# Kernel optimization log

Hardware: AMD Instinct MI355X
Metric: run time of the kernel (lower is better)

The kernel has to match this reference:

```python
import jax, jax.numpy as jnp
import numpy as np
import math

H = 16
D_MODEL = 1024
D_K = D_MODEL // H


def setup_inputs() -> dict:
    key = jax.random.key(0)
    ks = jax.random.split(key, 12)
    B, S = 4, 2048
    inp = {
        "query": jax.random.normal(ks[0], (B, S, D_MODEL), jnp.float32),
        "key": jax.random.normal(ks[1], (B, S, D_MODEL), jnp.float32),
        "value": jax.random.normal(ks[2], (B, S, D_MODEL), jnp.float32),
        # causal mask, broadcastable over heads: [B, 1, S, S]
        "mask": jnp.broadcast_to(jnp.tril(jnp.ones((S, S), bool)), (B, 1, S, S)),
    }
    sc = 1.0 / math.sqrt(D_MODEL)
    inp["Wq"] = jax.random.normal(ks[3], (D_MODEL, D_MODEL), jnp.float32) * sc
    inp["bq"] = jnp.zeros((D_MODEL,), jnp.float32)
    inp["Wk"] = jax.random.normal(ks[4], (D_MODEL, D_MODEL), jnp.float32) * sc
    inp["bk"] = jnp.zeros((D_MODEL,), jnp.float32)
    inp["Wv"] = jax.random.normal(ks[5], (D_MODEL, D_MODEL), jnp.float32) * sc
    inp["bv"] = jnp.zeros((D_MODEL,), jnp.float32)
    inp["Wo"] = jax.random.normal(ks[6], (D_MODEL, D_MODEL), jnp.float32) * sc
    inp["bo"] = jnp.zeros((D_MODEL,), jnp.float32)
    return inp


def reference(query, key, value, mask, Wq, bq, Wk, bk, Wv, bv, Wo, bo):
    B, S, D = query.shape
    # torch nn.Linear: y = x @ W.T + b; then view(B,-1,h,d_k).transpose(1,2)
    def proj(x, W, b):
        return (x @ W.T + b).reshape(B, -1, H, D_K).transpose(0, 2, 1, 3)  # [B,h,S,d_k]

    q = proj(query, Wq, bq)
    k = proj(key, Wk, bk)
    v = proj(value, Wv, bv)

    scores = jnp.einsum("bhqd,bhkd->bhqk", q, k) / math.sqrt(D_K)
    scores = jnp.where(mask, scores, jnp.finfo(scores.dtype).min)
    p_attn = jax.nn.softmax(scores, axis=-1)  # dropout: eval mode (identity)
    x = jnp.einsum("bhqk,bhkd->bhqd", p_attn, v)
    x = x.transpose(0, 2, 1, 3).reshape(B, -1, H * D_K)
    return x @ Wo.T + bo
```

## Files before the change

kernel.cpp:

```cpp
#include <hip/hip_runtime.h>
#include <hip/hip_bf16.h>

typedef unsigned short u16;
typedef unsigned int u32;
typedef __attribute__((ext_vector_type(8))) short short8;
typedef __attribute__((ext_vector_type(4))) short short4v;
typedef __attribute__((ext_vector_type(4))) float f32x4;
typedef __attribute__((ext_vector_type(4))) float float4_t;

#define DIM 1024
#define NH  16
#define DKK 64
#define SEQ 2048
#define NB  4
#define SM_SCALE 0.1803368801111244f

__device__ __forceinline__ u16 f2bf(float f) {
    __bf16 h = (__bf16)f;
    return __builtin_bit_cast(u16, h);
}

__device__ __forceinline__ f32x4 mfma_bf16(short8 a, short8 b, f32x4 c) {
    return __builtin_amdgcn_mfma_f32_16x16x32_bf16(a, b, c, 0, 0, 0);
}

__device__ __forceinline__ short8 pack8(float4_t a, float4_t b) {
    short8 v;
    v[0] = (short)f2bf(a[0]); v[1] = (short)f2bf(a[1]);
    v[2] = (short)f2bf(a[2]); v[3] = (short)f2bf(a[3]);
    v[4] = (short)f2bf(b[0]); v[5] = (short)f2bf(b[1]);
    v[6] = (short)f2bf(b[2]); v[7] = (short)f2bf(b[3]);
    return v;
}

typedef const __attribute__((address_space(1))) u32* gas1_t;
typedef __attribute__((address_space(3))) u32* las3_t;
__device__ __forceinline__ void g2l16(const void* g, void* l) {
    __builtin_amdgcn_global_load_lds((gas1_t)g, (las3_t)l, 16, 0, 0);
}

template<int MODE>
__global__ __launch_bounds__(256)
void gemm128(const float* __restrict__ Afp, const u16* __restrict__ Abf,
             const float* __restrict__ W, const float* __restrict__ bias,
             u16* __restrict__ Cbf, float* __restrict__ Cf)
{
    __shared__ __align__(16) char AsRaw[MODE == 1 ? 8192 : 16384];
    __shared__ __align__(16) float Bs[128 * 32];

    const int tid  = threadIdx.x;
    const int lane = tid & 63;
    const int w    = tid >> 6;
    const int wr   = w >> 1, wc = w & 1;
    const int m0   = blockIdx.y * 128;
    const int n0   = blockIdx.x * 128;
    const int lm   = lane & 15, lg = lane >> 4;

    const int fr = tid >> 3;
    const int fc = (tid & 7) ^ ((tid >> 3) & 7);
    const int hr = tid >> 2;
    const int hc = (tid & 3) ^ ((tid >> 3) & 3);

    f32x4 acc[4][4];
#pragma unroll
    for (int i = 0; i < 4; ++i)
#pragma unroll
        for (int j = 0; j < 4; ++j) acc[i][j] = (f32x4){0.f, 0.f, 0.f, 0.f};

    for (int k0 = 0; k0 < DIM; k0 += 32) {
        __syncthreads();
        if (MODE == 1) {
#pragma unroll
            for (int c = 0; c < 2; ++c)
                g2l16(Abf + (size_t)(m0 + c * 64 + hr) * DIM + k0 + hc * 8,
                      AsRaw + c * 4096 + w * 1024);
        } else {
#pragma unroll
            for (int c = 0; c < 4; ++c)
                g2l16(Afp + (size_t)(m0 + c * 32 + fr) * DIM + k0 + fc * 4,
                      AsRaw + c * 4096 + w * 1024);
        }
#pragma unroll
        for (int c = 0; c < 4; ++c)
            g2l16(W + (size_t)(n0 + c * 32 + fr) * DIM + k0 + fc * 4,
                  (char*)Bs + c * 4096 + w * 1024);
        __syncthreads();

        short8 af[4], bfr[4];
#pragma unroll
        for (int t = 0; t < 4; ++t) {
            {
                const int R = wc * 64 + t * 16 + lm;
                const float* rowp = Bs + R * 32;
                const int sw = lm & 7;
                const float4_t fa = *(const float4_t*)(rowp + ((((lg * 2)    ) ^ sw) << 2));
                const float4_t fb = *(const float4_t*)(rowp + ((((lg * 2) | 1) ^ sw) << 2));
                bfr[t] = pack8(fa, fb);
            }
            const int R = wr * 64 + t * 16 + lm;
            if (MODE == 1) {
                const u16* Ash = (const u16*)AsRaw;
                const int ch = lg ^ ((lm >> 1) & 3);
                af[t] = *(const short8*)(Ash + R * 32 + ch * 8);
            } else {
                const float* Asf = (const float*)AsRaw;
                const float* rowp = Asf + R * 32;
                const int sw = lm & 7;
                const float4_t fa = *(const float4_t*)(rowp + ((((lg * 2)    ) ^ sw) << 2));
                const float4_t fb = *(const float4_t*)(rowp + ((((lg * 2) | 1) ^ sw) << 2));
                af[t] = pack8(fa, fb);
            }
        }
#pragma unroll
        for (int mt = 0; mt < 4; ++mt)
#pragma unroll
            for (int nt = 0; nt < 4; ++nt)
                acc[mt][nt] = mfma_bf16(af[mt], bfr[nt], acc[mt][nt]);
    }

#pragma unroll
    for (int mt = 0; mt < 4; ++mt)
#pragma unroll
        for (int nt = 0; nt < 4; ++nt)
#pragma unroll
            for (int r = 0; r < 4; ++r) {
                const int m = m0 + wr * 64 + mt * 16 + lg * 4 + r;
                const int n = n0 + wc * 64 + nt * 16 + lm;
                if (MODE == 0) {
                    const float val = acc[mt][nt][r] + bias[n];
                    const int b = m >> 11, s = m & 2047;
                    const int h = n >> 6,  dk = n & 63;
                    Cbf[(((size_t)b * NH + h) * SEQ + s) * DKK + dk] = f2bf(val);
                } else if (MODE == 1) {
                    Cf[(size_t)m * DIM + n] = acc[mt][nt][r] + bias[n];
                } else {
                    const float val = acc[mt][nt][r] + bias[m];
                    const int h = m >> 6, dk = m & 63;
                    const int b = n >> 11, s = n & 2047;
                    Cbf[(((size_t)b * NH + h) * DKK + dk) * SEQ + s] = f2bf(val);
                }
            }
}

__global__ __launch_bounds__(256, 2)
void attn3(const u16* __restrict__ Q, const u16* __restrict__ K,
           const u16* __restrict__ Vt, u16* __restrict__ O)
{
    __shared__ __align__(16) u16 Ks[64][72];
    __shared__ __align__(16) u16 Vs[64][72];
    __shared__ __align__(16) u16 Ps[4][32][72];

    const int tid  = threadIdx.x;
    const int lane = tid & 63;
    const int w    = tid >> 6;
    const int lm   = lane & 15, lg = lane >> 4;
    const int Lr   = blockIdx.y * gridDim.x + blockIdx.x;
    const int work = (Lr & 7) * 128 + (Lr >> 3);
    const int pb   = work & 15;
    const int bh   = work >> 4;
    const int Abase = pb * 64;
    const int Bbase = SEQ - 64 - Abase;
    const int qA = Abase + 16 * w;
    const int qB = Bbase + 16 * w;
    const u16* Qp = Q  + (size_t)bh * SEQ * DKK;
    const u16* Kp = K  + (size_t)bh * SEQ * DKK;
    const u16* Vp = Vt + (size_t)bh * DKK * SEQ;

    short8 qa[2][2];
#pragma unroll
    for (int kh = 0; kh < 2; ++kh) {
        qa[0][kh] = *(const short8*)(Qp + (size_t)(qA + lm) * DKK + kh * 32 + lg * 8);
        qa[1][kh] = *(const short8*)(Qp + (size_t)(qB + lm) * DKK + kh * 32 + lg * 8);
    }

    float m_q[2] = {-INFINITY, -INFINITY};
    float l_q[2] = {0.f, 0.f};
    f32x4 o[2][4];
#pragma unroll
    for (int qt = 0; qt < 2; ++qt)
#pragma unroll
        for (int dt = 0; dt < 4; ++dt) o[qt][dt] = (f32x4){0.f, 0.f, 0.f, 0.f};

    const f32x4 zero = (f32x4){0.f, 0.f, 0.f, 0.f};
    const int srow = tid >> 3;
    const int soct = (tid & 7) * 8;
    const int kv_end = Bbase + 64;

    short8 rk0 = *(const short8*)(Kp + (size_t)srow * DKK + soct);
    short8 rk1 = *(const short8*)(Kp + (size_t)(srow + 32) * DKK + soct);
    short8 rv0 = *(const short8*)(Vp + (size_t)srow * SEQ + soct);
    short8 rv1 = *(const short8*)(Vp + (size_t)(srow + 32) * SEQ + soct);

    for (int kv0 = 0; kv0 < kv_end; kv0 += 64) {
        __syncthreads();
        *(short8*)&Ks[srow][soct]      = rk0;
        *(short8*)&Ks[srow + 32][soct] = rk1;
        *(short8*)&Vs[srow][soct]      = rv0;
        *(short8*)&Vs[srow + 32][soct] = rv1;
        const int nkv = kv0 + 64;
        if (nkv < kv_end) {
            rk0 = *(const short8*)(Kp + (size_t)(nkv + srow) * DKK + soct);
            rk1 = *(const short8*)(Kp + (size_t)(nkv + srow + 32) * DKK + soct);
            rv0 = *(const short8*)(Vp + (size_t)srow * SEQ + nkv + soct);
            rv1 = *(const short8*)(Vp + (size_t)(srow + 32) * SEQ + nkv + soct);
        }
        __syncthreads();

        const bool actA = kv0 < qA + 16;
        const bool msk[2] = { kv0 + 63 > qA, kv0 + 63 > qB };
        const bool act[2] = { actA, true };
        const int  qb[2]  = { qA, qB };

        f32x4 s[2][4];
#pragma unroll
        for (int kvt = 0; kvt < 4; ++kvt) {
            const short8 kb0 = *(const short8*)&Ks[kvt * 16 + lm][lg * 8];
            const short8 kb1 = *(const short8*)&Ks[kvt * 16 + lm][32 + lg * 8];
            s[1][kvt] = mfma_bf16(kb1, qa[1][1], mfma_bf16(kb0, qa[1][0], zero));
            if (actA)
                s[0][kvt] = mfma_bf16(kb1, qa[0][1], mfma_bf16(kb0, qa[0][0], zero));
        }

        float mx[2] = {-INFINITY, -INFINITY};
#pragma unroll
        for (int qt = 0; qt < 2; ++qt) {
            if (!act[qt]) continue;
#pragma unroll
            for (int kvt = 0; kvt < 4; ++kvt)
#pragma unroll
                for (int r = 0; r < 4; ++r) s[qt][kvt][r] *= SM_SCALE;
            if (msk[qt]) {
                const int q = qb[qt] + lm;
#pragma unroll
                for (int kvt = 0; kvt < 4; ++kvt)
#pragma unroll
                    for (int r = 0; r < 4; ++r) {
                        const int kv = kv0 + kvt * 16 + lg * 4 + r;
                        if (kv > q) s[qt][kvt][r] = -INFINITY;
                    }
            }
            float vmax = -INFINITY;
#pragma unroll
            for (int kvt = 0; kvt < 4; ++kvt)
#pragma unroll
                for (int r = 0; r < 4; ++r) vmax = fmaxf(vmax, s[qt][kvt][r]);
            vmax = fmaxf(vmax, __shfl_xor(vmax, 16));
            vmax = fmaxf(vmax, __shfl_xor(vmax, 32));
            mx[qt] = vmax;
        }

        const bool small = (!actA || mx[0] <= m_q[0] + 8.f) && (mx[1] <= m_q[1] + 8.f);
        if (__all(small)) {
#pragma unroll
            for (int qt = 0; qt < 2; ++qt) {
                if (!act[qt]) continue;
                float ls = 0.f;
#pragma unroll
                for (int kvt = 0; kvt < 4; ++kvt) {
                    short4v pk;
#pragma unroll
                    for (int r = 0; r < 4; ++r) {
                        const float p = __builtin_exp2f(s[qt][kvt][r] - m_q[qt]);
                        ls += p;
                        pk[r] = (short)f2bf(p);
                    }
                    *(short4v*)&Ps[w][qt * 16 + lm][kvt * 16 + lg * 4] = pk;
                }
                l_q[qt] += ls;
            }
        } else {
#pragma unroll
            for (int qt = 0; qt < 2; ++qt) {
                if (!act[qt]) continue;
                const float mnew = fmaxf(m_q[qt], mx[qt]);
                const float alpha = __builtin_exp2f(m_q[qt] - mnew);
                m_q[qt] = mnew;
                float ls = 0.f;
#pragma unroll
                for (int kvt = 0; kvt < 4; ++kvt) {
                    short4v pk;
#pragma unroll
                    for (int r = 0; r < 4; ++r) {
                        const float p = __builtin_exp2f(s[qt][kvt][r] - mnew);
                        ls += p;
                        pk[r] = (short)f2bf(p);
                    }
                    *(short4v*)&Ps[w][qt * 16 + lm][kvt * 16 + lg * 4] = pk;
                }
                l_q[qt] = l_q[qt] * alpha + ls;
#pragma unroll
                for (int r = 0; r < 4; ++r) {
                    const float ar = __shfl(alpha, lg * 4 + r);
#pragma unroll
                    for (int dt = 0; dt < 4; ++dt) o[qt][dt][r] *= ar;
                }
            }
        }
        asm volatile("s_waitcnt lgkmcnt(0)" ::: "memory");

        short8 pa[2][2], vbt[4][2];
#pragma unroll
        for (int qt = 0; qt < 2; ++qt)
            if (act[qt]) {
                pa[qt][0] = *(const short8*)&Ps[w][qt * 16 + lm][lg * 8];
                pa[qt][1] = *(const short8*)&Ps[w][qt * 16 + lm][32 + lg * 8];
            }
#pragma unroll
        for (int dt = 0; dt < 4; ++dt) {
            vbt[dt][0] = *(const short8*)&Vs[dt * 16 + lm][lg * 8];
            vbt[dt][1] = *(const short8*)&Vs[dt * 16 + lm][32 + lg * 8];
        }
#pragma unroll
        for (int dt = 0; dt < 4; ++dt)
#pragma unroll
            for (int qt = 0; qt < 2; ++qt) {
                if (!act[qt]) continue;
                o[qt][dt] = mfma_bf16(pa[qt][1], vbt[dt][1],
                                      mfma_bf16(pa[qt][0], vbt[dt][0], o[qt][dt]));
            }
    }

    const int b = bh >> 4, h = bh & 15;
#pragma unroll
    for (int qt = 0; qt < 2; ++qt) {
        float lf = l_q[qt];
        lf += __shfl_xor(lf, 16);
        lf += __shfl_xor(lf, 32);
        const int qbase = qt ? qB : qA;
#pragma unroll
        for (int r = 0; r < 4; ++r) {
            const float li = 1.f / __shfl(lf, lg * 4 + r);
            const int srw = qbase + lg * 4 + r;
#pragma unroll
            for (int dt = 0; dt < 4; ++dt)
                O[(((size_t)b * SEQ + srw) * NH + h) * DKK + dt * 16 + lm] =
                    f2bf(o[qt][dt][r] * li);
        }
    }
}

extern "C" void kernel_launch(void* const* d_in, const int* in_sizes, int n_in,
                              void* d_out, int out_size, void* d_ws, size_t ws_size,
                              hipStream_t stream)
{
    const float* query = (const float*)d_in[0];
    const float* key   = (const float*)d_in[1];
    const float* value = (const float*)d_in[2];
    const float* Wq = (const float*)d_in[4];
    const float* bq = (const float*)d_in[5];
    const float* Wk = (const float*)d_in[6];
    const float* bk = (const float*)d_in[7];
    const float* Wv = (const float*)d_in[8];
    const float* bv = (const float*)d_in[9];
    const float* Wo = (const float*)d_in[10];
    const float* bo = (const float*)d_in[11];
    float* out = (float*)d_out;

    const size_t HD = (size_t)NB * NH * SEQ * DKK;
    u16* qws  = (u16*)d_ws;
    u16* kws  = qws + HD;
    u16* vtws = kws + HD;
    u16* ows  = vtws + HD;

    dim3 gg(DIM / 128, (NB * SEQ) / 128);
    dim3 gv((NB * SEQ) / 128, DIM / 128);
    gemm128<0><<<gg, 256, 0, stream>>>(query, nullptr, Wq, bq, qws, nullptr);
    gemm128<0><<<gg, 256, 0, stream>>>(key,   nullptr, Wk, bk, kws, nullptr);
    gemm128<2><<<gv, 256, 0, stream>>>(Wv, nullptr, value, bv, vtws, nullptr);
    attn3<<<dim3(16, NB * NH), 256, 0, stream>>>(qws, kws, vtws, ows);
    gemm128<1><<<gg, 256, 0, stream>>>(nullptr, ows, Wo, bo, nullptr, out);
}
```

Before: 264.6 us.

## Pre-convert inputs and weights to bf16 before GEMMs and fold softmax scale into Q

```diff
diff --git a/kernel.cpp b/kernel.cpp
--- a/kernel.cpp
+++ b/kernel.cpp
@@ -39,15 +39,43 @@
     __builtin_amdgcn_global_load_lds((gas1_t)g, (las3_t)l, 16, 0, 0);
 }
 
+__device__ __forceinline__ float max16(const f32x4* s) {
+    const float a = fmaxf(fmaxf(s[0][0], s[0][1]), fmaxf(s[0][2], s[0][3]));
+    const float b = fmaxf(fmaxf(s[1][0], s[1][1]), fmaxf(s[1][2], s[1][3]));
+    const float c = fmaxf(fmaxf(s[2][0], s[2][1]), fmaxf(s[2][2], s[2][3]));
+    const float d = fmaxf(fmaxf(s[3][0], s[3][1]), fmaxf(s[3][2], s[3][3]));
+    return fmaxf(fmaxf(a, b), fmaxf(c, d));
+}
+
+__global__ __launch_bounds__(256) void conv8(const float* __restrict__ src,
+                                             u16* __restrict__ dst) {
+    const int i = (blockIdx.x * 256 + threadIdx.x) * 8;
+    const float4_t a = *(const float4_t*)(src + i);
+    const float4_t b = *(const float4_t*)(src + i + 4);
+    *(short8*)(dst + i) = pack8(a, b);
+}
+
+__global__ __launch_bounds__(256) void conv8w(const float* __restrict__ w0,
+                                              const float* __restrict__ w1,
+                                              const float* __restrict__ w2,
+                                              const float* __restrict__ w3,
+                                              u16* __restrict__ dst) {
+    const int t = blockIdx.y;
+    const float* s = t == 0 ? w0 : t == 1 ? w1 : t == 2 ? w2 : w3;
+    const int i = (blockIdx.x * 256 + threadIdx.x) * 8;
+    const float4_t a = *(const float4_t*)(s + i);
+    const float4_t b = *(const float4_t*)(s + i + 4);
+    *(short8*)(dst + (size_t)t * DIM * DIM + i) = pack8(a, b);
+}
+
 template<int MODE>
 __global__ __launch_bounds__(256)
-void gemm128(const float* __restrict__ Afp, const u16* __restrict__ Abf,
-             const float* __restrict__ W, const float* __restrict__ bias,
-             u16* __restrict__ Cbf, float* __restrict__ Cf)
+void gemmb(const u16* __restrict__ A, const u16* __restrict__ Bw,
+           const float* __restrict__ bias, float scale,
+           u16* __restrict__ Cbf, float* __restrict__ Cf)
 {
-    __shared__ __align__(16) char AsRaw[MODE == 1 ? 8192 : 16384];
-    __shared__ __align__(16) float Bs[128 * 32];
-
+    __shared__ __align__(16) u16 As[128][32];
+    __shared__ __align__(16) u16 Bs[128][32];
     const int tid  = threadIdx.x;
     const int lane = tid & 63;
     const int w    = tid >> 6;
@@ -55,11 +83,8 @@
     const int m0   = blockIdx.y * 128;
     const int n0   = blockIdx.x * 128;
     const int lm   = lane & 15, lg = lane >> 4;
-
-    const int fr = tid >> 3;
-    const int fc = (tid & 7) ^ ((tid >> 3) & 7);
-    const int hr = tid >> 2;
-    const int hc = (tid & 3) ^ ((tid >> 3) & 3);
+    const int srow = lane >> 2;
+    const int scol = (lane & 3) * 8;
 
     f32x4 acc[4][4];
 #pragma unroll
@@ -69,47 +94,20 @@
 
     for (int k0 = 0; k0 < DIM; k0 += 32) {
         __syncthreads();
-        if (MODE == 1) {
-#pragma unroll
-            for (int c = 0; c < 2; ++c)
-                g2l16(Abf + (size_t)(m0 + c * 64 + hr) * DIM + k0 + hc * 8,
-                      AsRaw + c * 4096 + w * 1024);
-        } else {
-#pragma unroll
-            for (int c = 0; c < 4; ++c)
-                g2l16(Afp + (size_t)(m0 + c * 32 + fr) * DIM + k0 + fc * 4,
-                      AsRaw + c * 4096 + w * 1024);
-        }
-#pragma unroll
-        for (int c = 0; c < 4; ++c)
-            g2l16(W + (size_t)(n0 + c * 32 + fr) * DIM + k0 + fc * 4,
-                  (char*)Bs + c * 4096 + w * 1024);
+#pragma unroll
+        for (int i = 0; i < 2; ++i) {
+            g2l16(A  + (size_t)(m0 + w * 32 + i * 16 + srow) * DIM + k0 + scol,
+                  &As[w * 32 + i * 16][0]);
+            g2l16(Bw + (size_t)(n0 + w * 32 + i * 16 + srow) * DIM + k0 + scol,
+                  &Bs[w * 32 + i * 16][0]);
+        }
         __syncthreads();
 
         short8 af[4], bfr[4];
 #pragma unroll
         for (int t = 0; t < 4; ++t) {
-            {
-                const int R = wc * 64 + t * 16 + lm;
-                const float* rowp = Bs + R * 32;
-                const int sw = lm & 7;
-                const float4_t fa = *(const float4_t*)(rowp + ((((lg * 2)    ) ^ sw) << 2));
-                const float4_t fb = *(const float4_t*)(rowp + ((((lg * 2) | 1) ^ sw) << 2));
-                bfr[t] = pack8(fa, fb);
-            }
-            const int R = wr * 64 + t * 16 + lm;
-            if (MODE == 1) {
-                const u16* Ash = (const u16*)AsRaw;
-                const int ch = lg ^ ((lm >> 1) & 3);
-                af[t] = *(const short8*)(Ash + R * 32 + ch * 8);
-            } else {
-                const float* Asf = (const float*)AsRaw;
-                const float* rowp = Asf + R * 32;
-                const int sw = lm & 7;
-                const float4_t fa = *(const float4_t*)(rowp + ((((lg * 2)    ) ^ sw) << 2));
-                const float4_t fb = *(const float4_t*)(rowp + ((((lg * 2) | 1) ^ sw) << 2));
-                af[t] = pack8(fa, fb);
-            }
+            af[t]  = *(const short8*)&As[wr * 64 + t * 16 + lm][lg * 8];
+            bfr[t] = *(const short8*)&Bs[wc * 64 + t * 16 + lm][lg * 8];
         }
 #pragma unroll
         for (int mt = 0; mt < 4; ++mt)
@@ -127,7 +125,7 @@
                 const int m = m0 + wr * 64 + mt * 16 + lg * 4 + r;
                 const int n = n0 + wc * 64 + nt * 16 + lm;
                 if (MODE == 0) {
-                    const float val = acc[mt][nt][r] + bias[n];
+                    const float val = (acc[mt][nt][r] + bias[n]) * scale;
                     const int b = m >> 11, s = m & 2047;
                     const int h = n >> 6,  dk = n & 63;
                     Cbf[(((size_t)b * NH + h) * SEQ + s) * DKK + dk] = f2bf(val);
@@ -225,10 +223,6 @@
 #pragma unroll
         for (int qt = 0; qt < 2; ++qt) {
             if (!act[qt]) continue;
-#pragma unroll
-            for (int kvt = 0; kvt < 4; ++kvt)
-#pragma unroll
-                for (int r = 0; r < 4; ++r) s[qt][kvt][r] *= SM_SCALE;
             if (msk[qt]) {
                 const int q = qb[qt] + lm;
 #pragma unroll
@@ -239,11 +233,7 @@
                         if (kv > q) s[qt][kvt][r] = -INFINITY;
                     }
             }
-            float vmax = -INFINITY;
-#pragma unroll
-            for (int kvt = 0; kvt < 4; ++kvt)
-#pragma unroll
-                for (int r = 0; r < 4; ++r) vmax = fmaxf(vmax, s[qt][kvt][r]);
+            float vmax = max16(s[qt]);
             vmax = fmaxf(vmax, __shfl_xor(vmax, 16));
             vmax = fmaxf(vmax, __shfl_xor(vmax, 32));
             mx[qt] = vmax;
@@ -254,19 +244,20 @@
 #pragma unroll
             for (int qt = 0; qt < 2; ++qt) {
                 if (!act[qt]) continue;
-                float ls = 0.f;
+                float part[4];
 #pragma unroll
                 for (int kvt = 0; kvt < 4; ++kvt) {
                     short4v pk;
+                    f32x4 p;
 #pragma unroll
                     for (int r = 0; r < 4; ++r) {
-                        const float p = __builtin_exp2f(s[qt][kvt][r] - m_q[qt]);
-                        ls += p;
-                        pk[r] = (short)f2bf(p);
+                        p[r] = __builtin_exp2f(s[qt][kvt][r] - m_q[qt]);
+                        pk[r] = (short)f2bf(p[r]);
                     }
+                    part[kvt] = (p[0] + p[1]) + (p[2] + p[3]);
                     *(short4v*)&Ps[w][qt * 16 + lm][kvt * 16 + lg * 4] = pk;
                 }
-                l_q[qt] += ls;
+                l_q[qt] += (part[0] + part[1]) + (part[2] + part[3]);
             }
         } else {
 #pragma unroll
@@ -275,19 +266,20 @@
                 const float mnew = fmaxf(m_q[qt], mx[qt]);
                 const float alpha = __builtin_exp2f(m_q[qt] - mnew);
                 m_q[qt] = mnew;
-                float ls = 0.f;
+                float part[4];
 #pragma unroll
                 for (int kvt = 0; kvt < 4; ++kvt) {
                     short4v pk;
+                    f32x4 p;
 #pragma unroll
                     for (int r = 0; r < 4; ++r) {
-                        const float p = __builtin_exp2f(s[qt][kvt][r] - mnew);
-                        ls += p;
-                        pk[r] = (short)f2bf(p);
+                        p[r] = __builtin_exp2f(s[qt][kvt][r] - mnew);
+                        pk[r] = (short)f2bf(p[r]);
                     }
+                    part[kvt] = (p[0] + p[1]) + (p[2] + p[3]);
                     *(short4v*)&Ps[w][qt * 16 + lm][kvt * 16 + lg * 4] = pk;
                 }
-                l_q[qt] = l_q[qt] * alpha + ls;
+                l_q[qt] = l_q[qt] * alpha + (part[0] + part[1]) + (part[2] + part[3]);
 #pragma unroll
                 for (int r = 0; r < 4; ++r) {
                     const float ar = __shfl(alpha, lg * 4 + r);
@@ -357,16 +349,26 @@
     float* out = (float*)d_out;
 
     const size_t HD = (size_t)NB * NH * SEQ * DKK;
+    const size_t WSZ = (size_t)DIM * DIM;
     u16* qws  = (u16*)d_ws;
     u16* kws  = qws + HD;
     u16* vtws = kws + HD;
     u16* ows  = vtws + HD;
+    u16* wbf  = ows + HD;
+    u16* cvt  = ows;
 
     dim3 gg(DIM / 128, (NB * SEQ) / 128);
     dim3 gv((NB * SEQ) / 128, DIM / 128);
-    gemm128<0><<<gg, 256, 0, stream>>>(query, nullptr, Wq, bq, qws, nullptr);
-    gemm128<0><<<gg, 256, 0, stream>>>(key,   nullptr, Wk, bk, kws, nullptr);
-    gemm128<2><<<gv, 256, 0, stream>>>(Wv, nullptr, value, bv, vtws, nullptr);
+    const int ca = (int)(HD / 2048);
+    conv8w<<<dim3(WSZ / 2048, 4), 256, 0, stream>>>(Wq, Wk, Wv, Wo, wbf);
+
+    conv8<<<ca, 256, 0, stream>>>(query, cvt);
+    gemmb<0><<<gg, 256, 0, stream>>>(cvt, wbf, bq, SM_SCALE, qws, nullptr);
+    conv8<<<ca, 256, 0, stream>>>(key, cvt);
+    gemmb<0><<<gg, 256, 0, stream>>>(cvt, wbf + WSZ, bk, 1.f, kws, nullptr);
+    conv8<<<ca, 256, 0, stream>>>(value, cvt);
+    gemmb<2><<<gv, 256, 0, stream>>>(wbf + 2 * WSZ, cvt, bv, 1.f, vtws, nullptr);
+
     attn3<<<dim3(16, NB * NH), 256, 0, stream>>>(qws, kws, vtws, ows);
-    gemm128<1><<<gg, 256, 0, stream>>>(nullptr, ows, Wo, bo, nullptr, out);
-}
+    gemmb<1><<<gg, 256, 0, stream>>>(ows, wbf + 3 * WSZ, bo, 1.f, nullptr, out);
+}
```

Result: faster. 245.9 us (-7.1%).
